# Performance work log

Hardware: AMD Instinct MI355X
Metric: run time of the kernel (lower is better)

Reference implementation:

```python
import math
import jax, jax.numpy as jnp
import numpy as np

PHI = (1.0 + math.sqrt(5.0)) / 2.0
LUT_N = 4096
TWO_PI = 2.0 * math.pi


def _lut_tables():
    angles = jnp.arange(LUT_N, dtype=jnp.float32) * (TWO_PI / LUT_N)
    return jnp.sin(angles), jnp.cos(angles)


def _lut_sin_cos(theta, sin_t, cos_t):
    # quantize angle to nearest LUT entry, wrap mod 2*pi
    idx = jnp.mod(jnp.round(theta * (LUT_N / TWO_PI)).astype(jnp.int32), LUT_N)
    return jnp.take(sin_t, idx), jnp.take(cos_t, idx)


def setup_inputs() -> dict:
    key = jax.random.key(0)
    ks = jax.random.split(key, 8)
    B, D, H = 4096, 4096, 16
    Dh = D // H
    return {
        'x_real': jax.random.normal(ks[0], (B, D), dtype=jnp.float32),
        'x_imag': jax.random.normal(ks[1], (B, D), dtype=jnp.float32),
        't': jax.random.uniform(ks[2], (B,), dtype=jnp.float32) * 100.0,
        'trigger_real': jax.random.normal(ks[3], (H, Dh), dtype=jnp.float32) * 0.5,
        'trigger_imag': jax.random.normal(ks[4], (H, Dh), dtype=jnp.float32) * 0.5,
        'w_query': jax.random.normal(ks[5], (H, Dh), dtype=jnp.float32) * 0.02,
        'b_query': jnp.zeros((H, Dh), dtype=jnp.float32),
        'w_out': jax.random.normal(ks[6], (D,), dtype=jnp.float32) * 0.02,
        'b_out': jnp.zeros((D,), dtype=jnp.float32),
        'beta': jnp.abs(jax.random.normal(ks[7], (D,), dtype=jnp.float32)) * 5.0 + 5.0,
    }


def reference(x_real, x_imag, t, trigger_real, trigger_imag, w_query, b_query, w_out, b_out, beta):
    sin_t, cos_t = _lut_tables()
    B, D = x_real.shape
    H, Dh = trigger_real.shape

    # ---- per-head interference (vectorized over heads) ----
    xr = x_real.reshape(B, H, Dh)
    xi = x_imag.reshape(B, H, Dh)
    t_phi_h = (t * PHI)[:, None, None]                       # (B,1,1)
    wavelength_q = 1.0 + jnp.abs(w_query)                    # (H,Dh)
    theta_r = xr / wavelength_q + b_query + t_phi_h
    theta_i = xi / wavelength_q + b_query + t_phi_h
    sin_r, cos_r = _lut_sin_cos(theta_r, sin_t, cos_t)
    sin_i, cos_i = _lut_sin_cos(theta_i, sin_t, cos_t)
    q_real = cos_r * cos_i - sin_r * sin_i                   # (B,H,Dh)
    q_imag = cos_r * sin_i + sin_r * cos_i
    int_r = (q_real * trigger_real + q_imag * trigger_imag).sum(-1)   # (B,H)
    int_i = (q_real * trigger_imag - q_imag * trigger_real).sum(-1)
    total_int_real = int_r.mean(-1)                          # (B,)
    total_int_imag = int_i.mean(-1)

    # ---- constant-Q memory update (fresh memory = zeros) ----
    beta_eff = 1.0 / (1.0 + jnp.abs(beta))                   # (D,)
    w_eff = 1.0 / (1.0 + jnp.abs(w_out))                     # (D,)
    decay = jnp.minimum(jnp.exp(-beta_eff * w_eff), 0.9999)
    int_mag = jnp.sqrt(total_int_real ** 2 + total_int_imag ** 2 + 1e-8)[:, None]  # (B,1)
    write_scale = (w_eff * (1.0 - decay))[None, :]           # (1,D)
    # initial memory is zero -> memory*decay term vanishes
    mem_real = x_real * int_mag * write_scale
    mem_imag = x_imag * int_mag * write_scale

    # ---- Euler projection of memory ----
    wavelength = 1.0 + jnp.abs(w_out)
    t_phi = (t * PHI)[:, None]
    th_or = mem_real / wavelength + b_out + t_phi
    th_oi = mem_imag / wavelength + b_out + t_phi
    sin_or, cos_or = _lut_sin_cos(th_or, sin_t, cos_t)
    sin_oi, cos_oi = _lut_sin_cos(th_oi, sin_t, cos_t)
    out_real = cos_or * cos_oi - sin_or * sin_oi
    out_imag = cos_or * sin_oi + sin_or * cos_oi
    return out_real, out_imag
```

## Files before the change

### kernel.cpp

```cpp
#include <hip/hip_runtime.h>

#define LUT_N 4096
#define DVAL  4096
#define TPB   512

static constexpr double TWO_PI_D = 6.283185307179586476925286766559;
#define PHI_F 1.61803398874989484820f

typedef float f32x4_t __attribute__((ext_vector_type(4)));

__device__ __forceinline__ float fc(const float4& f, int j) {
    switch (j) { case 0: return f.x; case 1: return f.y; case 2: return f.z; }
    return f.w;
}
__device__ __forceinline__ void sc4(float4& f, int j, float v) {
    switch (j) { case 0: f.x = v; return; case 1: f.y = v; return; case 2: f.z = v; return; }
    f.w = v;
}
__device__ __forceinline__ int lut_round(float theta, float cidx) {
    return (int)rintf(theta * cidx);
}
__device__ __forceinline__ void nt_store4(float4 v, float4* p) {
    f32x4_t w; w.x = v.x; w.y = v.y; w.z = v.z; w.w = v.w;
    __builtin_nontemporal_store(w, (f32x4_t*)p);
}

__global__ __launch_bounds__(256) void echo_precompute(
    const float* __restrict__ w_query,
    const float* __restrict__ w_out,
    const float* __restrict__ beta,
    float2* __restrict__ lut,
    float*  __restrict__ invq,
    float*  __restrict__ wsi)
{
    int i = blockIdx.x * 256 + threadIdx.x;
    const float c2 = (float)(TWO_PI_D / (double)LUT_N);
    if (i < LUT_N) {
        float ang = (float)i * c2;
        lut[i] = make_float2(sinf(ang), cosf(ang));
    }
    if (i < DVAL) {
        float inv_q     = 1.0f / (1.0f + fabsf(w_query[i]));
        float w_eff     = 1.0f / (1.0f + fabsf(w_out[i]));
        float beta_eff  = 1.0f / (1.0f + fabsf(beta[i]));
        float decay     = fminf(expf(-beta_eff * w_eff), 0.9999f);
        invq[i] = inv_q;
        wsi[i]  = (w_eff * (1.0f - decay)) * w_eff;
    }
}

template<bool USE_WS>
__global__ __launch_bounds__(TPB, 8) void echo_main(
    const float* __restrict__ x_real,
    const float* __restrict__ x_imag,
    const float* __restrict__ t,
    const float* __restrict__ trig_r,
    const float* __restrict__ trig_i,
    const float* __restrict__ w_query,
    const float* __restrict__ b_query,
    const float* __restrict__ w_out,
    const float* __restrict__ b_out,
    const float* __restrict__ beta,
    const float2* __restrict__ lutG,
    const float*  __restrict__ invqG,
    const float*  __restrict__ wsiG,
    float* __restrict__ out,
    int B)
{
    __shared__ float2 lutS[LUT_N];
    __shared__ float redR[8], redI[8];
    __shared__ float magS[2];

    const int tid  = threadIdx.x;
    const int half = tid >> 8;
    const int lane = tid & 255;
    int row = blockIdx.x * 2 + half;
    if (row >= B) row = B - 1;
    const float cidx = (float)((double)LUT_N / TWO_PI_D);

    if constexpr (USE_WS) {
        const float4* src = (const float4*)lutG;
        float4* dst = (float4*)lutS;
        #pragma unroll
        for (int k = 0; k < 4; ++k) {
            int idx = tid + TPB * k;
            dst[idx] = src[idx];
        }
    } else {
        const float c2 = (float)(TWO_PI_D / (double)LUT_N);
        #pragma unroll
        for (int k = 0; k < 8; ++k) {
            int idx = tid + TPB * k;
            float ang = (float)idx * c2;
            lutS[idx] = make_float2(sinf(ang), cosf(ang));
        }
    }

    const float tphi = t[row] * PHI_F;
    const float* xr = x_real + (size_t)row * DVAL;
    const float* xi = x_imag + (size_t)row * DVAL;

    float4 xr_s[4], xi_s[4];
    float accr = 0.0f, acci = 0.0f;

    __syncthreads();

    #pragma unroll
    for (int k = 0; k < 4; ++k) {
        int v = lane + 256 * k;
        float4 a = ((const float4*)xr)[v];
        float4 c = ((const float4*)xi)[v];
        xr_s[k] = a; xi_s[k] = c;

        float4 iv4;
        if constexpr (USE_WS) {
            iv4 = ((const float4*)invqG)[v];
        } else {
            float4 wq4 = ((const float4*)w_query)[v];
            iv4 = make_float4(1.0f / (1.0f + fabsf(wq4.x)), 1.0f / (1.0f + fabsf(wq4.y)),
                              1.0f / (1.0f + fabsf(wq4.z)), 1.0f / (1.0f + fabsf(wq4.w)));
        }
        float4 bq4 = ((const float4*)b_query)[v];
        float4 tr4 = ((const float4*)trig_r)[v];
        float4 ti4 = ((const float4*)trig_i)[v];

        #pragma unroll
        for (int j = 0; j < 4; ++j) {
            float iv = fc(iv4, j), bq = fc(bq4, j);
            float thr = __builtin_fmaf(fc(a, j), iv, bq) + tphi;
            float thi = __builtin_fmaf(fc(c, j), iv, bq) + tphi;
            int idx = (lut_round(thr, cidx) + lut_round(thi, cidx)) & (LUT_N - 1);
            float2 s = lutS[idx];
            float q_r = s.y, q_i = s.x;
            accr = __builtin_fmaf(q_r, fc(tr4, j), __builtin_fmaf(q_i, fc(ti4, j), accr));
            acci = __builtin_fmaf(q_r, fc(ti4, j), __builtin_fmaf(-q_i, fc(tr4, j), acci));
        }
    }

    #pragma unroll
    for (int m = 32; m >= 1; m >>= 1) {
        accr += __shfl_xor(accr, m, 64);
        acci += __shfl_xor(acci, m, 64);
    }
    const int wave = tid >> 6;
    if ((tid & 63) == 0) { redR[wave] = accr; redI[wave] = acci; }
    __syncthreads();
    if (lane == 0) {
        int o = half * 4;
        float tr = (redR[o] + redR[o+1] + redR[o+2] + redR[o+3]) * 0.0625f;
        float ti = (redI[o] + redI[o+1] + redI[o+2] + redI[o+3]) * 0.0625f;
        magS[half] = sqrtf(tr * tr + ti * ti + 1e-8f);
    }
    __syncthreads();
    const float mag = magS[half];

    float4* outR = (float4*)(out + (size_t)row * DVAL);
    float4* outI = (float4*)(out + (size_t)B * DVAL + (size_t)row * DVAL);

    #pragma unroll
    for (int k = 0; k < 4; ++k) {
        int v = lane + 256 * k;
        float4 ws4;
        if constexpr (USE_WS) {
            ws4 = ((const float4*)wsiG)[v];
        } else {
            float4 wo4 = ((const float4*)w_out)[v];
            float4 be4 = ((const float4*)beta)[v];
            #pragma unroll
            for (int j = 0; j < 4; ++j) {
                float w_eff = 1.0f / (1.0f + fabsf(fc(wo4, j)));
                float beta_eff = 1.0f / (1.0f + fabsf(fc(be4, j)));
                float decay = fminf(expf(-beta_eff * w_eff), 0.9999f);
                sc4(ws4, j, (w_eff * (1.0f - decay)) * w_eff);
            }
        }
        float4 bo4 = ((const float4*)b_out)[v];

        float4 oR, oI;
        #pragma unroll
        for (int j = 0; j < 4; ++j) {
            float wsi_j = fc(ws4, j), bo = fc(bo4, j);
            float xmr = fc(xr_s[k], j) * mag;
            float xmi = fc(xi_s[k], j) * mag;
            float thr = __builtin_fmaf(xmr, wsi_j, bo) + tphi;
            float thi = __builtin_fmaf(xmi, wsi_j, bo) + tphi;
            int idx = (lut_round(thr, cidx) + lut_round(thi, cidx)) & (LUT_N - 1);
            float2 s = lutS[idx];
            sc4(oR, j, s.y);
            sc4(oI, j, s.x);
        }
        nt_store4(oR, &outR[v]);
        nt_store4(oI, &outI[v]);
    }
}

extern "C" void kernel_launch(void* const* d_in, const int* in_sizes, int n_in,
                              void* d_out, int out_size, void* d_ws, size_t ws_size,
                              hipStream_t stream) {
    const float* x_real    = (const float*)d_in[0];
    const float* x_imag    = (const float*)d_in[1];
    const float* t         = (const float*)d_in[2];
    const float* trig_r    = (const float*)d_in[3];
    const float* trig_i    = (const float*)d_in[4];
    const float* w_query   = (const float*)d_in[5];
    const float* b_query   = (const float*)d_in[6];
    const float* w_out     = (const float*)d_in[7];
    const float* b_out     = (const float*)d_in[8];
    const float* beta      = (const float*)d_in[9];
    float* out = (float*)d_out;

    const int B = in_sizes[2];
    const int nblocks = (B + 1) / 2;
    const size_t need = (size_t)LUT_N * sizeof(float2) + 2 * (size_t)DVAL * sizeof(float);

    if (d_ws != nullptr && ws_size >= need) {
        char* ws = (char*)d_ws;
        float2* lut  = (float2*)ws;
        float*  invq = (float*)(ws + (size_t)LUT_N * sizeof(float2));
        float*  wsi  = invq + DVAL;
        echo_precompute<<<(LUT_N > DVAL ? LUT_N : DVAL) / 256, 256, 0, stream>>>(
            w_query, w_out, beta, lut, invq, wsi);
        echo_main<true><<<nblocks, TPB, 0, stream>>>(
            x_real, x_imag, t, trig_r, trig_i, w_query, b_query, w_out, b_out, beta,
            lut, invq, wsi, out, B);
    } else {
        echo_main<false><<<nblocks, TPB, 0, stream>>>(
            x_real, x_imag, t, trig_r, trig_i, w_query, b_query, w_out, b_out, beta,
            nullptr, nullptr, nullptr, out, B);
    }
}
```

Measured before the change: 260.6 us.

## Replace shared-memory sin/cos LUT with hardware sin/cos on quantized angle

The 4096-entry sin/cos table in LDS is removed. The combined quantized index is now turned into a fraction of a revolution, and the AMD hardware v_sin/v_cos instructions are called on it. This drops the per-block 32KB LDS fill and the random LDS gathers, and makes one row per 256-thread block possible, with plain stores replacing nontemporal ones. The risk is that hardware sin/cos may not exactly match the float32 table values at the quantized angles, and it adds transcendental ALU work per element.

```diff
diff --git a/kernel.cpp b/kernel.cpp
--- a/kernel.cpp
+++ b/kernel.cpp
@@ -2,12 +2,10 @@
 
 #define LUT_N 4096
 #define DVAL  4096
-#define TPB   512
+#define TPB   256
 
 static constexpr double TWO_PI_D = 6.283185307179586476925286766559;
 #define PHI_F 1.61803398874989484820f
-
-typedef float f32x4_t __attribute__((ext_vector_type(4)));
 
 __device__ __forceinline__ float fc(const float4& f, int j) {
     switch (j) { case 0: return f.x; case 1: return f.y; case 2: return f.z; }
@@ -17,28 +15,24 @@
     switch (j) { case 0: f.x = v; return; case 1: f.y = v; return; case 2: f.z = v; return; }
     f.w = v;
 }
-__device__ __forceinline__ int lut_round(float theta, float cidx) {
-    return (int)rintf(theta * cidx);
-}
-__device__ __forceinline__ void nt_store4(float4 v, float4* p) {
-    f32x4_t w; w.x = v.x; w.y = v.y; w.z = v.z; w.w = v.w;
-    __builtin_nontemporal_store(w, (f32x4_t*)p);
+__device__ __forceinline__ void grid_sincos(float thr, float thi, float cidx,
+                                            float& s_out, float& c_out) {
+    float r = rintf(thr * cidx);
+    float s = rintf(thi * cidx);
+    float rev = (r + s) * (1.0f / (float)LUT_N);
+    float frac = rev - floorf(rev);
+    s_out = __builtin_amdgcn_sinf(frac);
+    c_out = __builtin_amdgcn_cosf(frac);
 }
 
 __global__ __launch_bounds__(256) void echo_precompute(
     const float* __restrict__ w_query,
     const float* __restrict__ w_out,
     const float* __restrict__ beta,
-    float2* __restrict__ lut,
-    float*  __restrict__ invq,
-    float*  __restrict__ wsi)
+    float* __restrict__ invq,
+    float* __restrict__ wsi)
 {
     int i = blockIdx.x * 256 + threadIdx.x;
-    const float c2 = (float)(TWO_PI_D / (double)LUT_N);
-    if (i < LUT_N) {
-        float ang = (float)i * c2;
-        lut[i] = make_float2(sinf(ang), cosf(ang));
-    }
     if (i < DVAL) {
         float inv_q     = 1.0f / (1.0f + fabsf(w_query[i]));
         float w_eff     = 1.0f / (1.0f + fabsf(w_out[i]));
@@ -50,7 +44,7 @@
 }
 
 template<bool USE_WS>
-__global__ __launch_bounds__(TPB, 8) void echo_main(
+__global__ __launch_bounds__(TPB, 4) void echo_main(
     const float* __restrict__ x_real,
     const float* __restrict__ x_imag,
     const float* __restrict__ t,
@@ -61,40 +55,17 @@
     const float* __restrict__ w_out,
     const float* __restrict__ b_out,
     const float* __restrict__ beta,
-    const float2* __restrict__ lutG,
-    const float*  __restrict__ invqG,
-    const float*  __restrict__ wsiG,
+    const float* __restrict__ invqG,
+    const float* __restrict__ wsiG,
     float* __restrict__ out,
     int B)
 {
-    __shared__ float2 lutS[LUT_N];
-    __shared__ float redR[8], redI[8];
-    __shared__ float magS[2];
+    __shared__ float redR[4], redI[4];
+    __shared__ float magS;
 
-    const int tid  = threadIdx.x;
-    const int half = tid >> 8;
-    const int lane = tid & 255;
-    int row = blockIdx.x * 2 + half;
-    if (row >= B) row = B - 1;
+    const int tid = threadIdx.x;
+    const int row = blockIdx.x;
     const float cidx = (float)((double)LUT_N / TWO_PI_D);
-
-    if constexpr (USE_WS) {
-        const float4* src = (const float4*)lutG;
-        float4* dst = (float4*)lutS;
-        #pragma unroll
-        for (int k = 0; k < 4; ++k) {
-            int idx = tid + TPB * k;
-            dst[idx] = src[idx];
-        }
-    } else {
-        const float c2 = (float)(TWO_PI_D / (double)LUT_N);
-        #pragma unroll
-        for (int k = 0; k < 8; ++k) {
-            int idx = tid + TPB * k;
-            float ang = (float)idx * c2;
-            lutS[idx] = make_float2(sinf(ang), cosf(ang));
-        }
-    }
 
     const float tphi = t[row] * PHI_F;
     const float* xr = x_real + (size_t)row * DVAL;
@@ -103,11 +74,9 @@
     float4 xr_s[4], xi_s[4];
     float accr = 0.0f, acci = 0.0f;
 
-    __syncthreads();
-
     #pragma unroll
     for (int k = 0; k < 4; ++k) {
-        int v = lane + 256 * k;
+        int v = tid + TPB * k;
         float4 a = ((const float4*)xr)[v];
         float4 c = ((const float4*)xi)[v];
         xr_s[k] = a; xi_s[k] = c;
@@ -129,9 +98,8 @@
             float iv = fc(iv4, j), bq = fc(bq4, j);
             float thr = __builtin_fmaf(fc(a, j), iv, bq) + tphi;
             float thi = __builtin_fmaf(fc(c, j), iv, bq) + tphi;
-            int idx = (lut_round(thr, cidx) + lut_round(thi, cidx)) & (LUT_N - 1);
-            float2 s = lutS[idx];
-            float q_r = s.y, q_i = s.x;
+            float q_i, q_r;
+            grid_sincos(thr, thi, cidx, q_i, q_r);
             accr = __builtin_fmaf(q_r, fc(tr4, j), __builtin_fmaf(q_i, fc(ti4, j), accr));
             acci = __builtin_fmaf(q_r, fc(ti4, j), __builtin_fmaf(-q_i, fc(tr4, j), acci));
         }
@@ -142,24 +110,22 @@
         accr += __shfl_xor(accr, m, 64);
         acci += __shfl_xor(acci, m, 64);
     }
-    const int wave = tid >> 6;
-    if ((tid & 63) == 0) { redR[wave] = accr; redI[wave] = acci; }
+    if ((tid & 63) == 0) { redR[tid >> 6] = accr; redI[tid >> 6] = acci; }
     __syncthreads();
-    if (lane == 0) {
-        int o = half * 4;
-        float tr = (redR[o] + redR[o+1] + redR[o+2] + redR[o+3]) * 0.0625f;
-        float ti = (redI[o] + redI[o+1] + redI[o+2] + redI[o+3]) * 0.0625f;
-        magS[half] = sqrtf(tr * tr + ti * ti + 1e-8f);
+    if (tid == 0) {
+        float tr = (redR[0] + redR[1] + redR[2] + redR[3]) * 0.0625f;
+        float ti = (redI[0] + redI[1] + redI[2] + redI[3]) * 0.0625f;
+        magS = sqrtf(tr * tr + ti * ti + 1e-8f);
     }
     __syncthreads();
-    const float mag = magS[half];
+    const float mag = magS;
 
     float4* outR = (float4*)(out + (size_t)row * DVAL);
     float4* outI = (float4*)(out + (size_t)B * DVAL + (size_t)row * DVAL);
 
     #pragma unroll
     for (int k = 0; k < 4; ++k) {
-        int v = lane + 256 * k;
+        int v = tid + TPB * k;
         float4 ws4;
         if constexpr (USE_WS) {
             ws4 = ((const float4*)wsiG)[v];
@@ -184,13 +150,13 @@
             float xmi = fc(xi_s[k], j) * mag;
             float thr = __builtin_fmaf(xmr, wsi_j, bo) + tphi;
             float thi = __builtin_fmaf(xmi, wsi_j, bo) + tphi;
-            int idx = (lut_round(thr, cidx) + lut_round(thi, cidx)) & (LUT_N - 1);
-            float2 s = lutS[idx];
-            sc4(oR, j, s.y);
-            sc4(oI, j, s.x);
+            float s_o, c_o;
+            grid_sincos(thr, thi, cidx, s_o, c_o);
+            sc4(oR, j, c_o);
+            sc4(oI, j, s_o);
         }
-        nt_store4(oR, &outR[v]);
-        nt_store4(oI, &outI[v]);
+        outR[v] = oR;
+        outI[v] = oI;
     }
 }
 
@@ -210,22 +176,18 @@
     float* out = (float*)d_out;
 
     const int B = in_sizes[2];
-    const int nblocks = (B + 1) / 2;
-    const size_t need = (size_t)LUT_N * sizeof(float2) + 2 * (size_t)DVAL * sizeof(float);
+    const size_t need = 2 * (size_t)DVAL * sizeof(float);
 
     if (d_ws != nullptr && ws_size >= need) {
-        char* ws = (char*)d_ws;
-        float2* lut  = (float2*)ws;
-        float*  invq = (float*)(ws + (size_t)LUT_N * sizeof(float2));
-        float*  wsi  = invq + DVAL;
-        echo_precompute<<<(LUT_N > DVAL ? LUT_N : DVAL) / 256, 256, 0, stream>>>(
-            w_query, w_out, beta, lut, invq, wsi);
-        echo_main<true><<<nblocks, TPB, 0, stream>>>(
+        float* invq = (float*)d_ws;
+        float* wsi  = invq + DVAL;
+        echo_precompute<<<DVAL / 256, 256, 0, stream>>>(w_query, w_out, beta, invq, wsi);
+        echo_main<true><<<B, TPB, 0, stream>>>(
             x_real, x_imag, t, trig_r, trig_i, w_query, b_query, w_out, b_out, beta,
-            lut, invq, wsi, out, B);
+            invq, wsi, out, B);
     } else {
-        echo_main<false><<<nblocks, TPB, 0, stream>>>(
+        echo_main<false><<<B, TPB, 0, stream>>>(
             x_real, x_imag, t, trig_r, trig_i, w_query, b_query, w_out, b_out, beta,
-            nullptr, nullptr, nullptr, out, B);
+            nullptr, nullptr, out, B);
     }
 }
```

New measurement: 261.8 us. About the same (+0.5%).
